# Kernel optimization log

Hardware: AMD Instinct MI355X
Metric: run time of the kernel (lower is better)

## Reference

```python
import jax, jax.numpy as jnp
import numpy as np

N_HEADS = 4
N_HIDDEN = 128  # out_features, is_concat=False
NEG_SLOPE = 0.2


def setup_inputs() -> dict:
    key = jax.random.key(0)
    k1, k2, k3, k4 = jax.random.split(key, 4)
    A, S, P, F = 128, 64, 16, 128
    h = jax.random.normal(k1, (A, S, P, F), dtype=jnp.float32)
    # torch Linear(in, out, bias=False): y = x @ W.T ; here we store W already transposed [in, out]
    scale = 1.0 / np.sqrt(F)
    W_l = jax.random.normal(k2, (F, N_HEADS * N_HIDDEN), dtype=jnp.float32) * scale
    W_r = jax.random.normal(k3, (F, N_HEADS * N_HIDDEN), dtype=jnp.float32) * scale
    w_attn = jax.random.normal(k4, (2 * N_HIDDEN,), dtype=jnp.float32) * (1.0 / np.sqrt(2 * N_HIDDEN))
    return {"h": h, "W_l": W_l, "W_r": W_r, "w_attn": w_attn}


def reference(h, W_l, W_r, w_attn):
    A, S, P, F = h.shape
    H, D = N_HEADS, N_HIDDEN
    h_ = jnp.transpose(h, (1, 2, 0, 3))  # [S,P,A,F]
    g_l = (h_ @ W_l).reshape(S, P, A, H, D)
    g_r = (h_ @ W_r).reshape(S, P, A, H, D)
    # attn(cat(g_l[j], g_r[i])) = <w_attn[:D], g_l[j]> + <w_attn[D:], g_r[i]>
    # (single-output Linear over concat, shared across heads) — identical math,
    # avoids materializing the [S,P,A,A,H,2D] concat tensor.
    a_l, a_r = w_attn[:D], w_attn[D:]
    s_l = jnp.einsum('spahd,d->spah', g_l, a_l)  # contributes along j axis
    s_r = jnp.einsum('spahd,d->spah', g_r, a_r)  # contributes along i axis
    e = s_r[:, :, :, None, :] + s_l[:, :, None, :, :]  # [S,P,i,j,H]
    e = jax.nn.leaky_relu(e, negative_slope=NEG_SLOPE)
    diag = jnp.eye(A, dtype=bool)[None, None, :, :, None]  # mask self-edges
    e = jnp.where(diag, -jnp.inf, e)
    a = jax.nn.softmax(e, axis=3)  # softmax over j
    attn_res = jnp.einsum('spijh,spjhd->spihd', a, g_r)  # [S,P,A,H,D]
    attn_res = attn_res.mean(axis=3)  # is_concat=False -> mean over heads
    attn_res = jnp.transpose(attn_res, (2, 0, 1, 3))  # [A,S,P,D]
    return attn_res, a
```

## Files before the change

kernel.cpp:

```cpp
#include <hip/hip_runtime.h>
#include <hip/hip_bf16.h>
#include <stdint.h>


typedef short short8 __attribute__((ext_vector_type(8)));
typedef float f32x4 __attribute__((ext_vector_type(4)));

__device__ __forceinline__ float bf2f(unsigned short u) {
    return __uint_as_float(((unsigned int)u) << 16);
}
__device__ __forceinline__ unsigned short f2bf(float f) {
    unsigned int x = __float_as_uint(f);
    return (unsigned short)((x + 0x7FFFu + ((x >> 16) & 1u)) >> 16);
}
__device__ __forceinline__ float lrelu(float x) {
    return fmaxf(x, 0.2f * x);
}

__global__ void gat_precomp(const float* __restrict__ Wl,
                            const float* __restrict__ Wr,
                            const float* __restrict__ wattn,
                            unsigned short* __restrict__ Wt,
                            float* __restrict__ Vl,
                            float* __restrict__ Vr) {
    int b = blockIdx.x, t = threadIdx.x;
    if (b < 64) {
        int base = b * 1024 + t * 4;
        float4 v = *(const float4*)(Wr + base);
        int f = base >> 9;
        int c = base & 511;
        Wt[(c + 0) * 128 + f] = f2bf(v.x);
        Wt[(c + 1) * 128 + f] = f2bf(v.y);
        Wt[(c + 2) * 128 + f] = f2bf(v.z);
        Wt[(c + 3) * 128 + f] = f2bf(v.w);
    } else {
        const float* W  = (b == 64) ? Wl : Wr;
        const float* aw = wattn + ((b == 64) ? 0 : 128);
        float* V = (b == 64) ? Vl : Vr;
        for (int r = 0; r < 2; ++r) {
            int o = t + r * 256;
            int f = o >> 2, hh = o & 3;
            float acc = 0.f;
            for (int d = 0; d < 128; ++d)
                acc += W[f * 512 + hh * 128 + d] * aw[d];
            V[hh * 128 + f] = acc;
        }
    }
}

__global__ __launch_bounds__(512, 4)
void gat_main(const float* __restrict__ hin,
              const unsigned short* __restrict__ Wt,
              const float* __restrict__ Vl,
              const float* __restrict__ Vr,
              float* __restrict__ out_attn,
              float* __restrict__ out_a) {
    __shared__ __align__(16) unsigned short XG[2][128][136];
    __shared__ float sLs[4][128];
    __shared__ float sRs[4][128];
    __shared__ float Ms[4][128];
    __shared__ float Siv[4][128];

    const int sp = blockIdx.x;
    const int t = threadIdx.x;

    #pragma unroll
    for (int k = 0; k < 8; ++k) {
        int c = k * 512 + t;
        int a = c >> 5, cc = c & 31;
        float4 v = *(const float4*)(hin + (size_t)a * 131072 + sp * 128 + cc * 4);
        ushort4 uh, ul;
        uh.x = f2bf(v.x); ul.x = f2bf(v.x - bf2f(uh.x));
        uh.y = f2bf(v.y); ul.y = f2bf(v.y - bf2f(uh.y));
        uh.z = f2bf(v.z); ul.z = f2bf(v.z - bf2f(uh.z));
        uh.w = f2bf(v.w); ul.w = f2bf(v.w - bf2f(uh.w));
        *(ushort4*)(&XG[0][a][cc * 4]) = uh;
        *(ushort4*)(&XG[1][a][cc * 4]) = ul;
    }
    __syncthreads();

    {
        int a = t >> 2, hh = t & 3;
        float al = 0.f, ar = 0.f;
        for (int f = 0; f < 128; f += 4) {
            ushort4 xh = *(const ushort4*)(&XG[0][a][f]);
            ushort4 xl = *(const ushort4*)(&XG[1][a][f]);
            float4 vl = *(const float4*)(Vl + hh * 128 + f);
            float4 vr = *(const float4*)(Vr + hh * 128 + f);
            float x0 = bf2f(xh.x) + bf2f(xl.x);
            float x1 = bf2f(xh.y) + bf2f(xl.y);
            float x2 = bf2f(xh.z) + bf2f(xl.z);
            float x3 = bf2f(xh.w) + bf2f(xl.w);
            al += x0 * vl.x + x1 * vl.y + x2 * vl.z + x3 * vl.w;
            ar += x0 * vr.x + x1 * vr.y + x2 * vr.z + x3 * vr.w;
        }
        sLs[hh][a] = al;
        sRs[hh][a] = ar;
    }
    __syncthreads();

    {
        int i = t >> 2, hh = t & 3;
        float sr = sRs[hh][i];
        float m = -1e30f;
        for (int j = 0; j < 128; ++j) {
            if (j == i) continue;
            float e = lrelu(sr + sLs[hh][j]);
            m = fmaxf(m, e);
        }
        float sum = 0.f;
        for (int j = 0; j < 128; ++j) {
            if (j == i) continue;
            float e = lrelu(sr + sLs[hh][j]);
            sum += __expf(e - m);
        }
        Ms[hh][i] = m;
        Siv[hh][i] = 1.f / sum;
    }
    __syncthreads();

    const int w = t >> 6;
    const int l = t & 63;
    const int q = l >> 4;
    const int ln = l & 15;

    short8 axh[4], axl[4];
    #pragma unroll
    for (int kb = 0; kb < 4; ++kb) {
        axh[kb] = *(const short8*)(&XG[0][16 * w + ln][32 * kb + 8 * q]);
        axl[kb] = *(const short8*)(&XG[1][16 * w + ln][32 * kb + 8 * q]);
    }

    {
        float* oa = out_a + (size_t)sp * 65536;
        for (int k = 0; k < 32; ++k) {
            int idx = k * 512 + t;
            int i = idx >> 7, j = idx & 127;
            float4 r4;
            float* rp = (float*)&r4;
            #pragma unroll
            for (int hh = 0; hh < 4; ++hh) {
                float pv = 0.f;
                if (j != i) {
                    float e = lrelu(sRs[hh][i] + sLs[hh][j]);
                    pv = __expf(e - Ms[hh][i]) * Siv[hh][i];
                }
                rp[hh] = pv;
            }
            *(float4*)(oa + (size_t)idx * 4) = r4;
        }
    }

    f32x4 acc[8];
    #pragma unroll
    for (int tj = 0; tj < 8; ++tj) acc[tj] = (f32x4){0.f, 0.f, 0.f, 0.f};

    for (int hh = 0; hh < 4; ++hh) {
        __syncthreads();

        #pragma unroll
        for (int tj = 0; tj < 8; ++tj) {
            f32x4 g = (f32x4){0.f, 0.f, 0.f, 0.f};
            #pragma unroll
            for (int kb = 0; kb < 4; ++kb) {
                short8 bh = *(const short8*)(Wt + ((hh * 128 + 16 * tj + ln) * 128 + 32 * kb + 8 * q));
                g = __builtin_amdgcn_mfma_f32_16x16x32_bf16(axh[kb], bh, g, 0, 0, 0);
                g = __builtin_amdgcn_mfma_f32_16x16x32_bf16(axl[kb], bh, g, 0, 0, 0);
            }
            ushort4 gh4, gl4;
            unsigned short* ghp = (unsigned short*)&gh4;
            unsigned short* glp = (unsigned short*)&gl4;
            #pragma unroll
            for (int r = 0; r < 4; ++r) {
                float v = g[r];
                unsigned short hb = f2bf(v);
                ghp[r] = hb;
                glp[r] = f2bf(v - bf2f(hb));
            }
            *(ushort4*)(&XG[0][16 * tj + ln][16 * w + 4 * q]) = gh4;
            *(ushort4*)(&XG[1][16 * tj + ln][16 * w + 4 * q]) = gl4;
        }
        __syncthreads();

        {
            const int i = 16 * w + ln;
            const float sr = sRs[hh][i];
            const float m = Ms[hh][i];
            const float si = Siv[hh][i];
            #pragma unroll 1
            for (int kb = 0; kb < 4; ++kb) {
                short8 ph, pl;
                #pragma unroll
                for (int jj = 0; jj < 8; ++jj) {
                    int j = 32 * kb + 8 * q + jj;
                    float pv = 0.f;
                    if (j != i) {
                        float e = lrelu(sr + sLs[hh][j]);
                        pv = __expf(e - m) * si;
                    }
                    unsigned short hb = f2bf(pv);
                    ph[jj] = (short)hb;
                    pl[jj] = (short)f2bf(pv - bf2f(hb));
                }
                #pragma unroll
                for (int tj = 0; tj < 8; ++tj) {
                    short8 bh = *(const short8*)(&XG[0][16 * tj + ln][32 * kb + 8 * q]);
                    short8 bl = *(const short8*)(&XG[1][16 * tj + ln][32 * kb + 8 * q]);
                    acc[tj] = __builtin_amdgcn_mfma_f32_16x16x32_bf16(ph, bh, acc[tj], 0, 0, 0);
                    acc[tj] = __builtin_amdgcn_mfma_f32_16x16x32_bf16(ph, bl, acc[tj], 0, 0, 0);
                    acc[tj] = __builtin_amdgcn_mfma_f32_16x16x32_bf16(pl, bh, acc[tj], 0, 0, 0);
                }
            }
        }
    }

    #pragma unroll
    for (int tj = 0; tj < 8; ++tj) {
        int d = 16 * tj + ln;
        #pragma unroll
        for (int r = 0; r < 4; ++r) {
            int i = 16 * w + 4 * q + r;
            out_attn[((size_t)i * 1024 + sp) * 128 + d] = acc[tj][r] * 0.25f;
        }
    }
}

extern "C" void kernel_launch(void* const* d_in, const int* in_sizes, int n_in,
                              void* d_out, int out_size, void* d_ws, size_t ws_size,
                              hipStream_t stream) {
    const float* hin   = (const float*)d_in[0];
    const float* Wl    = (const float*)d_in[1];
    const float* Wr    = (const float*)d_in[2];
    const float* wattn = (const float*)d_in[3];

    unsigned short* Wt = (unsigned short*)d_ws;
    float* Vl = (float*)((char*)d_ws + 131072);
    float* Vr = (float*)((char*)d_ws + 131072 + 2048);

    float* out_attn = (float*)d_out;
    float* out_a    = (float*)d_out + 16777216;

    gat_precomp<<<66, 256, 0, stream>>>(Wl, Wr, wattn, Wt, Vl, Vr);
    gat_main<<<1024, 512, 0, stream>>>(hin, Wt, Vl, Vr, out_attn, out_a);
}
```

Measured before the change: 570.5 us.

## Drop split-bf16 low parts, compute scores from global h, use top-2 max trick

Removes the hi/lo bf16 split for the input features and the projected features, so each GEMM issues fewer MFMAs (one instead of two for the projection, two instead of three for aggregation). LDS shrinks to a single bf16 tile, which allows the launch bound to rise to 6 blocks per CU. The score dot products now read fp32 h directly from global memory. The per-row softmax max comes from a wave-level top-2 reduction of the left scores, using monotonicity of leaky-relu, instead of a separate max pass. The cost is lower precision in the projected features, plus repeated global loads of h inside the head loop.

```diff
diff --git a/kernel.cpp b/kernel.cpp
--- a/kernel.cpp
+++ b/kernel.cpp
@@ -48,88 +48,78 @@
     }
 }
 
-__global__ __launch_bounds__(512, 4)
+__global__ __launch_bounds__(512, 6)
 void gat_main(const float* __restrict__ hin,
               const unsigned short* __restrict__ Wt,
               const float* __restrict__ Vl,
               const float* __restrict__ Vr,
               float* __restrict__ out_attn,
               float* __restrict__ out_a) {
-    __shared__ __align__(16) unsigned short XG[2][128][136];
-    __shared__ float sLs[4][128];
-    __shared__ float sRs[4][128];
-    __shared__ float Ms[4][128];
-    __shared__ float Siv[4][128];
+    __shared__ __align__(16) unsigned short Gs[128][136];
+    __shared__ float sLs[4][132];
+    __shared__ float sRs[4][132];
+    __shared__ float Ms[4][132];
+    __shared__ float Siv[4][132];
+    __shared__ float mx1[4], mx2[4];
+    __shared__ int   ax1[4];
 
     const int sp = blockIdx.x;
     const int t = threadIdx.x;
-
-    #pragma unroll
-    for (int k = 0; k < 8; ++k) {
-        int c = k * 512 + t;
-        int a = c >> 5, cc = c & 31;
-        float4 v = *(const float4*)(hin + (size_t)a * 131072 + sp * 128 + cc * 4);
-        ushort4 uh, ul;
-        uh.x = f2bf(v.x); ul.x = f2bf(v.x - bf2f(uh.x));
-        uh.y = f2bf(v.y); ul.y = f2bf(v.y - bf2f(uh.y));
-        uh.z = f2bf(v.z); ul.z = f2bf(v.z - bf2f(uh.z));
-        uh.w = f2bf(v.w); ul.w = f2bf(v.w - bf2f(uh.w));
-        *(ushort4*)(&XG[0][a][cc * 4]) = uh;
-        *(ushort4*)(&XG[1][a][cc * 4]) = ul;
-    }
-    __syncthreads();
-
-    {
-        int a = t >> 2, hh = t & 3;
-        float al = 0.f, ar = 0.f;
-        for (int f = 0; f < 128; f += 4) {
-            ushort4 xh = *(const ushort4*)(&XG[0][a][f]);
-            ushort4 xl = *(const ushort4*)(&XG[1][a][f]);
-            float4 vl = *(const float4*)(Vl + hh * 128 + f);
-            float4 vr = *(const float4*)(Vr + hh * 128 + f);
-            float x0 = bf2f(xh.x) + bf2f(xl.x);
-            float x1 = bf2f(xh.y) + bf2f(xl.y);
-            float x2 = bf2f(xh.z) + bf2f(xl.z);
-            float x3 = bf2f(xh.w) + bf2f(xl.w);
-            al += x0 * vl.x + x1 * vl.y + x2 * vl.z + x3 * vl.w;
-            ar += x0 * vr.x + x1 * vr.y + x2 * vr.z + x3 * vr.w;
-        }
-        sLs[hh][a] = al;
-        sRs[hh][a] = ar;
-    }
-    __syncthreads();
-
-    {
-        int i = t >> 2, hh = t & 3;
-        float sr = sRs[hh][i];
-        float m = -1e30f;
-        for (int j = 0; j < 128; ++j) {
-            if (j == i) continue;
-            float e = lrelu(sr + sLs[hh][j]);
-            m = fmaxf(m, e);
-        }
-        float sum = 0.f;
-        for (int j = 0; j < 128; ++j) {
-            if (j == i) continue;
-            float e = lrelu(sr + sLs[hh][j]);
-            sum += __expf(e - m);
-        }
-        Ms[hh][i] = m;
-        Siv[hh][i] = 1.f / sum;
-    }
-    __syncthreads();
-
     const int w = t >> 6;
     const int l = t & 63;
     const int q = l >> 4;
     const int ln = l & 15;
 
-    short8 axh[4], axl[4];
-    #pragma unroll
-    for (int kb = 0; kb < 4; ++kb) {
-        axh[kb] = *(const short8*)(&XG[0][16 * w + ln][32 * kb + 8 * q]);
-        axl[kb] = *(const short8*)(&XG[1][16 * w + ln][32 * kb + 8 * q]);
-    }
+    {
+        int a = t >> 2, hh = t & 3;
+        const float* hr = hin + (size_t)a * 131072 + sp * 128;
+        const float* vl = Vl + hh * 128;
+        const float* vr = Vr + hh * 128;
+        float al = 0.f, ar = 0.f;
+        for (int f = 0; f < 128; f += 4) {
+            float4 x  = *(const float4*)(hr + f);
+            float4 a4 = *(const float4*)(vl + f);
+            float4 b4 = *(const float4*)(vr + f);
+            al += x.x * a4.x + x.y * a4.y + x.z * a4.z + x.w * a4.w;
+            ar += x.x * b4.x + x.y * b4.y + x.z * b4.z + x.w * b4.w;
+        }
+        sLs[hh][a] = al;
+        sRs[hh][a] = ar;
+    }
+    __syncthreads();
+
+    if (w < 4) {
+        float v0 = sLs[w][l], v1 = sLs[w][l + 64];
+        float m1, m2; int a1;
+        if (v0 >= v1) { m1 = v0; m2 = v1; a1 = l; }
+        else          { m1 = v1; m2 = v0; a1 = l + 64; }
+        #pragma unroll
+        for (int off = 32; off; off >>= 1) {
+            float o1 = __shfl_down(m1, off);
+            float o2 = __shfl_down(m2, off);
+            int   ob = __shfl_down(a1, off);
+            if (o1 > m1) { m2 = fmaxf(m1, o2); m1 = o1; a1 = ob; }
+            else         { m2 = fmaxf(m2, o1); }
+        }
+        if (l == 0) { mx1[w] = m1; mx2[w] = m2; ax1[w] = a1; }
+    }
+    __syncthreads();
+
+    {
+        int i = t >> 2, hh = t & 3;
+        float sr = sRs[hh][i];
+        float Mi = (i == ax1[hh]) ? mx2[hh] : mx1[hh];
+        float m = lrelu(sr + Mi);
+        float sum = 0.f;
+        for (int j = 0; j < 128; ++j) {
+            float e = lrelu(sr + sLs[hh][j]);
+            sum += __expf(e - m);
+        }
+        sum -= __expf(lrelu(sr + sLs[hh][i]) - m);
+        Ms[hh][i] = m;
+        Siv[hh][i] = 1.f / sum;
+    }
+    __syncthreads();
 
     {
         float* oa = out_a + (size_t)sp * 65536;
@@ -155,8 +145,23 @@
     #pragma unroll
     for (int tj = 0; tj < 8; ++tj) acc[tj] = (f32x4){0.f, 0.f, 0.f, 0.f};
 
+    const float* hrw = hin + (size_t)(16 * w + ln) * 131072 + sp * 128;
+
     for (int hh = 0; hh < 4; ++hh) {
         __syncthreads();
+
+        short8 axh[4];
+        #pragma unroll
+        for (int kb = 0; kb < 4; ++kb) {
+            float4 xa = *(const float4*)(hrw + 32 * kb + 8 * q);
+            float4 xb = *(const float4*)(hrw + 32 * kb + 8 * q + 4);
+            short8 v;
+            v[0] = (short)f2bf(xa.x); v[1] = (short)f2bf(xa.y);
+            v[2] = (short)f2bf(xa.z); v[3] = (short)f2bf(xa.w);
+            v[4] = (short)f2bf(xb.x); v[5] = (short)f2bf(xb.y);
+            v[6] = (short)f2bf(xb.z); v[7] = (short)f2bf(xb.w);
+            axh[kb] = v;
+        }
 
         #pragma unroll
         for (int tj = 0; tj < 8; ++tj) {
@@ -165,20 +170,12 @@
             for (int kb = 0; kb < 4; ++kb) {
                 short8 bh = *(const short8*)(Wt + ((hh * 128 + 16 * tj + ln) * 128 + 32 * kb + 8 * q));
                 g = __builtin_amdgcn_mfma_f32_16x16x32_bf16(axh[kb], bh, g, 0, 0, 0);
-                g = __builtin_amdgcn_mfma_f32_16x16x32_bf16(axl[kb], bh, g, 0, 0, 0);
             }
-            ushort4 gh4, gl4;
+            ushort4 gh4;
             unsigned short* ghp = (unsigned short*)&gh4;
-            unsigned short* glp = (unsigned short*)&gl4;
             #pragma unroll
-            for (int r = 0; r < 4; ++r) {
-                float v = g[r];
-                unsigned short hb = f2bf(v);
-                ghp[r] = hb;
-                glp[r] = f2bf(v - bf2f(hb));
-            }
-            *(ushort4*)(&XG[0][16 * tj + ln][16 * w + 4 * q]) = gh4;
-            *(ushort4*)(&XG[1][16 * tj + ln][16 * w + 4 * q]) = gl4;
+            for (int r = 0; r < 4; ++r) ghp[r] = f2bf(g[r]);
+            *(ushort4*)(&Gs[16 * tj + ln][16 * w + 4 * q]) = gh4;
         }
         __syncthreads();
 
@@ -204,10 +201,8 @@
                 }
                 #pragma unroll
                 for (int tj = 0; tj < 8; ++tj) {
-                    short8 bh = *(const short8*)(&XG[0][16 * tj + ln][32 * kb + 8 * q]);
-                    short8 bl = *(const short8*)(&XG[1][16 * tj + ln][32 * kb + 8 * q]);
+                    short8 bh = *(const short8*)(&Gs[16 * tj + ln][32 * kb + 8 * q]);
                     acc[tj] = __builtin_amdgcn_mfma_f32_16x16x32_bf16(ph, bh, acc[tj], 0, 0, 0);
-                    acc[tj] = __builtin_amdgcn_mfma_f32_16x16x32_bf16(ph, bl, acc[tj], 0, 0, 0);
                     acc[tj] = __builtin_amdgcn_mfma_f32_16x16x32_bf16(pl, bh, acc[tj], 0, 0, 0);
                 }
             }
```

Result: faster. 550.1 us (-3.6%).
